# Performance work log

Measured on AMD Instinct MI355X. Metric: run time of the kernel, lower is better.

Reference implementation:

```python
import jax, jax.numpy as jnp
import numpy as np

B, S = 512, 128            # batch_size, seq_len
NE, ED = 8192, 128         # num_edges, edge_dim
DD, ND = 32, 8             # direction_dim, num directions
H, PL = 512, 5             # hidden_dim, pre_len


def setup_inputs() -> dict:
    key = jax.random.key(0)
    ks = jax.random.split(key, 18)
    stdv = 1.0 / np.sqrt(64.0)
    u = lambda k, shp: jax.random.uniform(k, shp, jnp.float32, -stdv, stdv)
    inputs = jax.random.randint(ks[0], (B, S), 1, NE + 1)          # 1..num_edges
    directions = jax.random.randint(ks[1], (B, S), 1, ND + 1)      # 1..direction
    goal = jax.random.randint(ks[2], (B,), 0, NE)                  # 0..num_edges-1
    loc_dlabels_matrix = jax.random.randint(ks[3], (NE, NE), 0, ND)
    pred_d_rand = jax.random.uniform(ks[4], (B, ND * PL))
    link_emb_w = jax.random.normal(ks[5], (NE + 1, ED)) * 0.02
    link_emb_w = link_emb_w.at[0].set(0.0)  # padding_idx=0
    dir_emb_w = jax.random.normal(ks[6], (ND + 1, DD)) * 0.02
    dir_emb_w = dir_emb_w.at[0].set(0.0)
    w_ih = u(ks[7], (4 * H, ED + DD)); b_ih = u(ks[8], (4 * H,))
    w_hh = u(ks[9], (4 * H, H));       b_hh = u(ks[10], (4 * H,))
    W1 = jax.random.normal(ks[11], (H, H)) * 0.02; b1 = jnp.zeros((H,))
    W2 = jax.random.normal(ks[12], (H, H)) * 0.02; b2 = jnp.zeros((H,))
    W3 = jax.random.normal(ks[13], (ND, H)) * 0.02; b3 = jnp.zeros((ND,))
    return dict(inputs=inputs, directions=directions, goal=goal,
                loc_dlabels_matrix=loc_dlabels_matrix, pred_d_rand=pred_d_rand,
                link_emb_w=link_emb_w, dir_emb_w=dir_emb_w,
                w_ih=w_ih, b_ih=b_ih, w_hh=w_hh, b_hh=b_hh,
                W1=W1, b1=b1, W2=W2, b2=b2, W3=W3, b3=b3)


def _lstm_final_h(x_tbc, w_ih, b_ih, w_hh, b_hh):
    # x_tbc: (S, B, E); returns final hidden state (B, H)
    h0 = jnp.zeros((x_tbc.shape[1], H), x_tbc.dtype)
    c0 = jnp.zeros_like(h0)
    def step(carry, x_t):
        h, c = carry
        gates = x_t @ w_ih.T + b_ih + h @ w_hh.T + b_hh   # (B, 4H)
        i, f, g, o = jnp.split(gates, 4, axis=-1)
        c = jax.nn.sigmoid(f) * c + jax.nn.sigmoid(i) * jnp.tanh(g)
        h = jax.nn.sigmoid(o) * jnp.tanh(c)
        return (h, c), None
    (h, _), _ = jax.lax.scan(step, (h0, c0), x_tbc)
    return h


def reference(inputs, directions, goal, loc_dlabels_matrix, pred_d_rand,
              link_emb_w, dir_emb_w, w_ih, b_ih, w_hh, b_hh,
              W1, b1, W2, b2, W3, b3):
    last_obs = inputs[:, -1]
    # goal_directions_label - 1 (class target, 0..ND-1)
    lbl = loc_dlabels_matrix[last_obs - 1, goal]
    # edge-sequence embeddings: (B, S, ED+DD)
    x = jnp.concatenate([link_emb_w[inputs], dir_emb_w[directions]], axis=-1)
    h = _lstm_final_h(jnp.swapaxes(x, 0, 1), w_ih, b_ih, w_hh, b_hh)
    # dropout is identity at inference
    z = jax.nn.relu(h @ W1.T + b1)
    z = jax.nn.relu(z @ W2.T + b2)
    logits = z @ W3.T + b3                                # (B, ND)
    pred_d_prob = jax.nn.log_softmax(logits, axis=1)
    # torch CrossEntropyLoss re-applies log_softmax to pred_d_prob (faithful)
    ls2 = jax.nn.log_softmax(pred_d_prob, axis=1)
    loss = -jnp.mean(ls2[jnp.arange(B), lbl]) * 5.0
    _, idx = jax.lax.top_k(pred_d_prob, 2)                # (B, 2)
    direction_correct = jnp.sum(((idx[:, 0] == lbl) | (idx[:, 1] == lbl)).astype(jnp.int32))
    le = link_emb_w[last_obs]                             # (B, ED)
    de = dir_emb_w[idx + 1]                               # (B, 2, DD) -- only meaningful if DD==ED? no: added below
    query = le + 0.5 * (de[:, 0, :] + de[:, 1, :]) if ED == DD else le + 0.0 * le
    # NOTE: original code adds direction embeddings to link embedding; requires edge_dim==direction_dim?
    # In the source both are projected into the same space implicitly; here edge_dim != direction_dim,
    # so pad direction embedding to edge_dim with zeros to keep the same math shapewise.
    de_pad = jnp.pad(0.5 * (de[:, 0, :] + de[:, 1, :]), ((0, 0), (0, ED - DD)))
    query = le + de_pad
    sim = query @ link_emb_w[1:, :].T                     # (B, NE)
    pred_hard = jnp.tile(sim, (1, PL))                    # (B, NE*PL)
    return pred_hard, pred_d_rand, loss, direction_correct
```

## Files before the change

kernel.cpp:

```cpp
#include <hip/hip_runtime.h>
#include <stdint.h>


typedef __attribute__((ext_vector_type(8))) short short8;
typedef __attribute__((ext_vector_type(4))) float f32x4;

__device__ __forceinline__ unsigned short f2bf(float f) {
  union { float f; unsigned u; } v; v.f = f;
  return (unsigned short)((v.u + 0x7fffu + ((v.u >> 16) & 1u)) >> 16);
}
__device__ __forceinline__ float bf2f(unsigned short h) {
  union { unsigned u; float f; } v; v.u = ((unsigned)h) << 16;
  return v.f;
}
__device__ __forceinline__ f32x4 MFMA(short8 a, short8 b, f32x4 c) {
  return __builtin_amdgcn_mfma_f32_16x16x32_bf16(a, b, c, 0, 0, 0);
}

__global__ __launch_bounds__(256) void k_prep(
    const int* __restrict__ inputs, const int* __restrict__ dirs,
    const float* __restrict__ link, const float* __restrict__ dire,
    const float* __restrict__ w_ih, const float* __restrict__ w_hh,
    const float* __restrict__ W1, const float* __restrict__ W2,
    const float* __restrict__ W3, const float* __restrict__ b_ih,
    const float* __restrict__ b_hh,
    unsigned short* __restrict__ xb, unsigned short* __restrict__ wihb,
    unsigned short* __restrict__ whhb, unsigned short* __restrict__ w1b,
    unsigned short* __restrict__ w2b, unsigned short* __restrict__ w3b,
    unsigned short* __restrict__ linkb, float* __restrict__ bias_sum)
{
  int64_t e = (int64_t)blockIdx.x * 256 + threadIdx.x;
  if (e < 10485760) {
    int ei = (int)e;
    int s = ei / 81920;
    int r = ei % 81920;
    int b = r / 160, k = r % 160;
    float v;
    if (k < 128) v = link[(int64_t)inputs[b*128 + s]*128 + k];
    else         v = dire[dirs[b*128 + s]*32 + (k - 128)];
    xb[ei] = f2bf(v);
    return;
  }
  e -= 10485760;
  if (e < 327680)  { wihb[e] = f2bf(w_ih[e]); return; }
  e -= 327680;
  if (e < 1048576) { whhb[e] = f2bf(w_hh[e]); return; }
  e -= 1048576;
  if (e < 262144)  { w1b[e] = f2bf(W1[e]); return; }
  e -= 262144;
  if (e < 262144)  { w2b[e] = f2bf(W2[e]); return; }
  e -= 262144;
  if (e < 4096)    { w3b[e] = f2bf(W3[e]); return; }
  e -= 4096;
  if (e < 1048704) { linkb[e] = f2bf(link[e]); return; }
  e -= 1048704;
  if (e < 2048)    { bias_sum[e] = b_ih[e] + b_hh[e]; return; }
}

__global__ __launch_bounds__(256) void k_gatesx(
    const unsigned short* __restrict__ xb, const unsigned short* __restrict__ wihb,
    const float* __restrict__ bias_sum, unsigned short* __restrict__ gx)
{
  const int jt1 = blockIdx.x;
  const int bt2 = blockIdx.y;
  const int s   = blockIdx.z;
  const int t = threadIdx.x, w = t >> 6, l = t & 63;

  __shared__ unsigned short Ash[16*64*8];
  __shared__ unsigned short Bsh[8*64*8];

  f32x4 acc[4][8];
#pragma unroll
  for (int ns = 0; ns < 8; ns++) {
    int dj = ns >> 2, g = ns & 3;
    int gcol = 512*g + 32*jt1 + 16*dj + (l & 15);
    float bv = bias_sum[gcol];
    f32x4 b4; b4[0] = bv; b4[1] = bv; b4[2] = bv; b4[3] = bv;
#pragma unroll
    for (int msl = 0; msl < 4; msl++) acc[msl][ns] = b4;
  }
  const unsigned short* xrow = xb + (int64_t)(s*512 + bt2*256)*160;

  for (int ch = 0; ch < 5; ch++) {
    __syncthreads();
#pragma unroll
    for (int i = 0; i < 4; i++) {
      int slot = t + 256*i;
      int ms = slot >> 6, ll = slot & 63;
      int row = 16*ms + (ll & 15);
      int k = 32*ch + 8*(ll >> 4);
      *(uint4*)&Ash[slot*8] = *(const uint4*)&xrow[row*160 + k];
    }
#pragma unroll
    for (int i = 0; i < 2; i++) {
      int slot = t + 256*i;
      int ns = slot >> 6, ll = slot & 63;
      int dj = ns >> 2, g = ns & 3;
      int gcol = 512*g + 32*jt1 + 16*dj + (ll & 15);
      int k = 32*ch + 8*(ll >> 4);
      *(uint4*)&Bsh[slot*8] = *(const uint4*)&wihb[gcol*160 + k];
    }
    __syncthreads();
    short8 Bf[8];
#pragma unroll
    for (int ns = 0; ns < 8; ns++) Bf[ns] = *(short8*)&Bsh[(ns*64 + l)*8];
#pragma unroll
    for (int msl = 0; msl < 4; msl++) {
      short8 Af = *(short8*)&Ash[((4*w + msl)*64 + l)*8];
#pragma unroll
      for (int ns = 0; ns < 8; ns++)
        acc[msl][ns] = MFMA(Af, Bf[ns], acc[msl][ns]);
    }
  }
#pragma unroll
  for (int msl = 0; msl < 4; msl++) {
    int ms1 = 4*w + msl;
    int brow0 = 256*bt2 + 16*ms1;
    int bt = brow0 >> 6;
    int ms2 = (brow0 >> 4) & 3;
    int mw = ms2 >> 1, mt = ms2 & 1;
#pragma unroll
    for (int ns = 0; ns < 8; ns++) {
      int dj = ns >> 2, g = ns & 3;
      int jt2 = 2*jt1 + dj;
      int nw = g >> 1, nt = g & 1;
      int w2 = 2*nw + mw;
      int64_t idx = ((((((int64_t)s*32 + jt2)*8 + bt)*4 + w2)*2 + mt)*2 + nt)*64 + l;
      f32x4 a = acc[msl][ns];
      uint2 pk;
      unsigned short* ps = (unsigned short*)&pk;
      ps[0] = f2bf(a[0]); ps[1] = f2bf(a[1]); ps[2] = f2bf(a[2]); ps[3] = f2bf(a[3]);
      *(uint2*)&gx[idx*4] = pk;
    }
  }
}

__global__ __launch_bounds__(256) void k_lstm_step(
    const unsigned short* __restrict__ hprev, unsigned short* __restrict__ hnext,
    float* __restrict__ cbuf, const unsigned short* __restrict__ whhb,
    const unsigned short* __restrict__ gx, int s)
{
  const int jt = blockIdx.x;
  const int bt = blockIdx.y;
  const int t = threadIdx.x, w = t >> 6, l = t & 63;
  const int mw = w & 1, nw = w >> 1;

  __shared__ unsigned short Ash[4*2*64*8];
  __shared__ unsigned short Bsh[4*2*64*8];
  __shared__ float gsh[64][68];

  f32x4 acc[2][2];
#pragma unroll
  for (int mt = 0; mt < 2; mt++)
#pragma unroll
  for (int nt = 0; nt < 2; nt++) {
    int64_t idx = ((((((int64_t)s*32 + jt)*8 + bt)*4 + w)*2 + mt)*2 + nt)*64 + l;
    uint2 raw = *(const uint2*)(gx + idx*4);
    const unsigned short* pk = (const unsigned short*)&raw;
    f32x4 v;
    v[0] = bf2f(pk[0]); v[1] = bf2f(pk[1]); v[2] = bf2f(pk[2]); v[3] = bf2f(pk[3]);
    acc[mt][nt] = v;
  }

  for (int ch = 0; ch < 8; ch++) {
    __syncthreads();
#pragma unroll
    for (int i = 0; i < 2; i++) {
      int slot = t + 256*i;
      int p = slot >> 6, ll = slot & 63;
      int ms = p >> 1, ks = p & 1;
      int row = 64*bt + 16*ms + (ll & 15);
      int k = 64*ch + 32*ks + 8*(ll >> 4);
      *(uint4*)&Ash[slot*8] = *(const uint4*)&hprev[row*512 + k];
    }
#pragma unroll
    for (int i = 0; i < 2; i++) {
      int slot = t + 256*i;
      int p = slot >> 6, ll = slot & 63;
      int ns = p >> 1, ks = p & 1;
      int gcol = 512*ns + 16*jt + (ll & 15);
      int k = 64*ch + 32*ks + 8*(ll >> 4);
      *(uint4*)&Bsh[slot*8] = *(const uint4*)&whhb[gcol*512 + k];
    }
    __syncthreads();
#pragma unroll
    for (int ks = 0; ks < 2; ks++) {
      short8 A0 = *(short8*)&Ash[(((2*mw+0)*2 + ks)*64 + l)*8];
      short8 A1 = *(short8*)&Ash[(((2*mw+1)*2 + ks)*64 + l)*8];
      short8 B0 = *(short8*)&Bsh[(((2*nw+0)*2 + ks)*64 + l)*8];
      short8 B1 = *(short8*)&Bsh[(((2*nw+1)*2 + ks)*64 + l)*8];
      acc[0][0] = MFMA(A0, B0, acc[0][0]);
      acc[0][1] = MFMA(A0, B1, acc[0][1]);
      acc[1][0] = MFMA(A1, B0, acc[1][0]);
      acc[1][1] = MFMA(A1, B1, acc[1][1]);
    }
  }

#pragma unroll
  for (int mt = 0; mt < 2; mt++)
#pragma unroll
  for (int nt = 0; nt < 2; nt++) {
    int cb = 32*nw + 16*nt + (l & 15);
    int rb = 32*mw + 16*mt + (l >> 4)*4;
    f32x4 a = acc[mt][nt];
#pragma unroll
    for (int r = 0; r < 4; r++) gsh[rb + r][cb] = a[r];
  }
  __syncthreads();

  {
    int m = t >> 2, u0 = (t & 3)*4;
    int b = 64*bt + m;
    int j0 = 16*jt + u0;
    float* cp = cbuf + b*512 + j0;
    f32x4 c = *(f32x4*)cp;
    f32x4 cn;
    uint2 hv;
    unsigned short* hs = (unsigned short*)&hv;
#pragma unroll
    for (int i2 = 0; i2 < 4; i2++) {
      float gi = gsh[m][ 0 + u0 + i2];
      float gf = gsh[m][16 + u0 + i2];
      float gg = gsh[m][32 + u0 + i2];
      float go = gsh[m][48 + u0 + i2];
      float ii = 1.f/(1.f + expf(-gi));
      float ff = 1.f/(1.f + expf(-gf));
      float g2 = tanhf(gg);
      float oo = 1.f/(1.f + expf(-go));
      float cv = ff*c[i2] + ii*g2;
      cn[i2] = cv;
      hs[i2] = f2bf(oo * tanhf(cv));
    }
    *(f32x4*)cp = cn;
    *(uint2*)&hnext[b*512 + j0] = hv;
  }
}

__global__ __launch_bounds__(256, 1) void k_lstm_all(
    unsigned short* __restrict__ hb0, unsigned short* __restrict__ hb1,
    const unsigned short* __restrict__ whhb,
    const unsigned short* __restrict__ wihb,
    const unsigned short* __restrict__ xb,
    const float* __restrict__ bias_sum,
    unsigned int* __restrict__ flags)
{
  const int jt = blockIdx.x;
  const int bt = blockIdx.y;
  const int t = threadIdx.x, w = t >> 6, l = t & 63;
  const int mw = w & 1, nw = w >> 1;

  __shared__ unsigned short Ash[8*2*4*64*8];
  __shared__ float gsh[64][68];

  unsigned int* gf = flags + bt*32;

  short8 Bw[8][2][2];
#pragma unroll
  for (int ch = 0; ch < 8; ch++)
#pragma unroll
  for (int ks = 0; ks < 2; ks++)
#pragma unroll
  for (int nsl = 0; nsl < 2; nsl++) {
    int ns = 2*nw + nsl;
    int gcol = 512*ns + 16*jt + (l & 15);
    int k = 64*ch + 32*ks + 8*(l >> 4);
    Bw[ch][ks][nsl] = *(const short8*)&whhb[(int64_t)gcol*512 + k];
  }
  short8 Wx[5][2];
#pragma unroll
  for (int ch = 0; ch < 5; ch++)
#pragma unroll
  for (int nsl = 0; nsl < 2; nsl++) {
    int ns = 2*nw + nsl;
    int gcol = 512*ns + 16*jt + (l & 15);
    int k = 32*ch + 8*(l >> 4);
    Wx[ch][nsl] = *(const short8*)&wihb[(int64_t)gcol*160 + k];
  }
  float bias_b[2];
#pragma unroll
  for (int nt = 0; nt < 2; nt++) {
    int g = 2*nw + nt;
    bias_b[nt] = bias_sum[512*g + 16*jt + (l & 15)];
  }

  float creg[4] = {0.f, 0.f, 0.f, 0.f};
  const int m = t >> 2, u0 = (t & 3)*4;
  const int bgl = 64*bt + m;
  const int j0 = 16*jt + u0;

  short8 xf[2][5];
#pragma unroll
  for (int mt = 0; mt < 2; mt++)
#pragma unroll
  for (int ch = 0; ch < 5; ch++) {
    int row = 64*bt + 32*mw + 16*mt + (l & 15);
    int k = 32*ch + 8*(l >> 4);
    xf[mt][ch] = *(const short8*)&xb[(int64_t)(0*512 + row)*160 + k];
  }

  for (int s = 0; s < 128; s++) {
    const unsigned short* hp = (s & 1) ? hb1 : hb0;
    unsigned short* hn = (s & 1) ? hb0 : hb1;

    uint2 gxr[2][2];
#pragma unroll
    for (int mt = 0; mt < 2; mt++)
#pragma unroll
    for (int nt = 0; nt < 2; nt++) {
      f32x4 a;
      a[0] = bias_b[nt]; a[1] = bias_b[nt]; a[2] = bias_b[nt]; a[3] = bias_b[nt];
#pragma unroll
      for (int ch = 0; ch < 5; ch++)
        a = MFMA(xf[mt][ch], Wx[ch][nt], a);
      unsigned short* ps = (unsigned short*)&gxr[mt][nt];
      ps[0] = f2bf(a[0]); ps[1] = f2bf(a[1]); ps[2] = f2bf(a[2]); ps[3] = f2bf(a[3]);
    }

    {
      int sn = (s + 1 < 128) ? s + 1 : 127;
#pragma unroll
      for (int mt = 0; mt < 2; mt++)
#pragma unroll
      for (int ch = 0; ch < 5; ch++) {
        int row = 64*bt + 32*mw + 16*mt + (l & 15);
        int k = 32*ch + 8*(l >> 4);
        xf[mt][ch] = *(const short8*)&xb[(int64_t)(sn*512 + row)*160 + k];
      }
    }

    if (s > 0) {
      if (w == 0) {
        unsigned tgt = (unsigned)s;
        for (;;) {
          unsigned v = __hip_atomic_load(&gf[l & 31], __ATOMIC_RELAXED,
                                         __HIP_MEMORY_SCOPE_AGENT);
          if (__all((int)(v >= tgt))) break;
          __builtin_amdgcn_s_sleep(2);
        }
      }
      __syncthreads();
    }

#pragma unroll
    for (int i = 0; i < 16; i++) {
      int p = w*16 + i;
      int ms = p & 3, ks = (p >> 2) & 1, ch = p >> 3;
      int row = 64*bt + 16*ms + (l & 15);
      int k = 64*ch + 32*ks + 8*(l >> 4);
      const unsigned long long* src =
          (const unsigned long long*)(hp + (int64_t)row*512 + k);
      unsigned long long d0 = __hip_atomic_load(src,     __ATOMIC_RELAXED,
                                                __HIP_MEMORY_SCOPE_AGENT);
      unsigned long long d1 = __hip_atomic_load(src + 1, __ATOMIC_RELAXED,
                                                __HIP_MEMORY_SCOPE_AGENT);
      unsigned long long tmp[2] = {d0, d1};
      *(uint4*)&Ash[(p*64 + l)*8] = *(const uint4*)tmp;
    }
    __syncthreads();

    f32x4 acc[2][2];
#pragma unroll
    for (int mt = 0; mt < 2; mt++)
#pragma unroll
    for (int nt = 0; nt < 2; nt++) {
      const unsigned short* pk = (const unsigned short*)&gxr[mt][nt];
      f32x4 v;
      v[0] = bf2f(pk[0]); v[1] = bf2f(pk[1]); v[2] = bf2f(pk[2]); v[3] = bf2f(pk[3]);
      acc[mt][nt] = v;
    }

#pragma unroll
    for (int ch = 0; ch < 8; ch++)
#pragma unroll
    for (int ks = 0; ks < 2; ks++) {
      short8 A0 = *(short8*)&Ash[((ch*8 + ks*4 + 2*mw + 0)*64 + l)*8];
      short8 A1 = *(short8*)&Ash[((ch*8 + ks*4 + 2*mw + 1)*64 + l)*8];
      acc[0][0] = MFMA(A0, Bw[ch][ks][0], acc[0][0]);
      acc[0][1] = MFMA(A0, Bw[ch][ks][1], acc[0][1]);
      acc[1][0] = MFMA(A1, Bw[ch][ks][0], acc[1][0]);
      acc[1][1] = MFMA(A1, Bw[ch][ks][1], acc[1][1]);
    }

#pragma unroll
    for (int mt = 0; mt < 2; mt++)
#pragma unroll
    for (int nt = 0; nt < 2; nt++) {
      int cb = 32*nw + 16*nt + (l & 15);
      int rb = 32*mw + 16*mt + (l >> 4)*4;
      f32x4 a = acc[mt][nt];
#pragma unroll
      for (int r = 0; r < 4; r++) gsh[rb + r][cb] = a[r];
    }
    __syncthreads();

    {
      union { unsigned short hs[4]; unsigned long long v; } hv;
#pragma unroll
      for (int i2 = 0; i2 < 4; i2++) {
        float gi = gsh[m][ 0 + u0 + i2];
        float gf2 = gsh[m][16 + u0 + i2];
        float gg = gsh[m][32 + u0 + i2];
        float go = gsh[m][48 + u0 + i2];
        float ii = 1.f/(1.f + expf(-gi));
        float ff = 1.f/(1.f + expf(-gf2));
        float g2 = tanhf(gg);
        float oo = 1.f/(1.f + expf(-go));
        float cv = ff*creg[i2] + ii*g2;
        creg[i2] = cv;
        hv.hs[i2] = f2bf(oo * tanhf(cv));
      }
      __hip_atomic_store((unsigned long long*)&hn[(int64_t)bgl*512 + j0], hv.v,
                         __ATOMIC_RELAXED, __HIP_MEMORY_SCOPE_AGENT);
    }

    __syncthreads();
    if (t == 0) {
      asm volatile("s_waitcnt vmcnt(0)" ::: "memory");
      __hip_atomic_store(&gf[jt], (unsigned)(s + 1), __ATOMIC_RELAXED,
                         __HIP_MEMORY_SCOPE_AGENT);
    }
  }
}

template<int MODE>
__global__ __launch_bounds__(256) void k_gemm(
    const unsigned short* __restrict__ A, int lda,
    const unsigned short* __restrict__ Bm, int ldb, int nreal,
    const float* __restrict__ bias,
    void* __restrict__ outp, int ldo, int nchunks)
{
  const int bX = blockIdx.x, bY = blockIdx.y;
  const int t = threadIdx.x, w = t >> 6, l = t & 63;
  const int mw = w & 1, nw = w >> 1;
  __shared__ unsigned short Ash[4*2*64*8];
  __shared__ unsigned short Bsh[4*2*64*8];

  f32x4 acc[2][2];
  f32x4 z; z[0] = 0.f; z[1] = 0.f; z[2] = 0.f; z[3] = 0.f;
  acc[0][0] = z; acc[0][1] = z; acc[1][0] = z; acc[1][1] = z;

  for (int ch = 0; ch < nchunks; ch++) {
    __syncthreads();
#pragma unroll
    for (int i = 0; i < 2; i++) {
      int slot = t + 256*i;
      int p = slot >> 6, ll = slot & 63;
      int ms = p >> 1, ks = p & 1;
      int row = 64*bY + 16*ms + (ll & 15);
      int k = 64*ch + 32*ks + 8*(ll >> 4);
      *(uint4*)&Ash[slot*8] = *(const uint4*)&A[(int64_t)row*lda + k];
    }
#pragma unroll
    for (int i = 0; i < 2; i++) {
      int slot = t + 256*i;
      int p = slot >> 6, ll = slot & 63;
      int ns = p >> 1, ks = p & 1;
      int row = 64*bX + 16*ns + (ll & 15);
      if (row >= nreal) row = nreal - 1;
      int k = 64*ch + 32*ks + 8*(ll >> 4);
      *(uint4*)&Bsh[slot*8] = *(const uint4*)&Bm[(int64_t)row*ldb + k];
    }
    __syncthreads();
#pragma unroll
    for (int ks = 0; ks < 2; ks++) {
      short8 A0 = *(short8*)&Ash[(((2*mw+0)*2 + ks)*64 + l)*8];
      short8 A1 = *(short8*)&Ash[(((2*mw+1)*2 + ks)*64 + l)*8];
      short8 B0 = *(short8*)&Bsh[(((2*nw+0)*2 + ks)*64 + l)*8];
      short8 B1 = *(short8*)&Bsh[(((2*nw+1)*2 + ks)*64 + l)*8];
      acc[0][0] = MFMA(A0, B0, acc[0][0]);
      acc[0][1] = MFMA(A0, B1, acc[0][1]);
      acc[1][0] = MFMA(A1, B0, acc[1][0]);
      acc[1][1] = MFMA(A1, B1, acc[1][1]);
    }
  }

#pragma unroll
  for (int mt = 0; mt < 2; mt++)
#pragma unroll
  for (int nt = 0; nt < 2; nt++) {
    int n = 64*bX + 32*nw + 16*nt + (l & 15);
    int rb = 64*bY + 32*mw + 16*mt + (l >> 4)*4;
    f32x4 a = acc[mt][nt];
    if (MODE == 0) {
      float bv = bias[n];
#pragma unroll
      for (int r = 0; r < 4; r++) {
        float v = a[r] + bv; v = v > 0.f ? v : 0.f;
        ((unsigned short*)outp)[(int64_t)(rb + r)*ldo + n] = f2bf(v);
      }
    } else if (MODE == 1) {
      if (n < nreal) {
        float bv = bias[n];
#pragma unroll
        for (int r = 0; r < 4; r++)
          ((float*)outp)[(int64_t)(rb + r)*ldo + n] = a[r] + bv;
      }
    } else {
#pragma unroll
      for (int r = 0; r < 4; r++) {
        float v = a[r];
        float* o = (float*)outp + (int64_t)(rb + r)*40960 + n;
#pragma unroll
        for (int p5 = 0; p5 < 5; p5++) o[p5*8192] = v;
      }
    }
  }
}

__global__ __launch_bounds__(256) void k_head(
    const float* __restrict__ logits, const int* __restrict__ inputs,
    const int* __restrict__ goal, const int* __restrict__ ldm,
    const float* __restrict__ link, const float* __restrict__ dire,
    const float* __restrict__ pdr, unsigned short* __restrict__ qb,
    float* __restrict__ out)
{
  const int blk = blockIdx.x, t = threadIdx.x;
  __shared__ int idxsh[64][2];
  __shared__ float redf[256];
  __shared__ int redi[256];

  if (t < 64) {
    int b = 64*blk + t;
    float v[8];
#pragma unroll
    for (int i = 0; i < 8; i++) v[i] = logits[b*8 + i];
    int i0 = 0; float m0 = v[0];
#pragma unroll
    for (int i = 1; i < 8; i++) if (v[i] > m0) { m0 = v[i]; i0 = i; }
    int i1 = -1; float m1 = -3.4e38f;
#pragma unroll
    for (int i = 0; i < 8; i++) if (i != i0 && v[i] > m1) { m1 = v[i]; i1 = i; }
    idxsh[t][0] = i0; idxsh[t][1] = i1;
  }
  __syncthreads();
  {
    int rl = t >> 2, kc = (t & 3) * 32;
    int b = 64*blk + rl;
    int last = inputs[b*128 + 127];
    const float* le = link + (int64_t)last*128 + kc;
    int i0 = idxsh[rl][0], i1 = idxsh[rl][1];
    unsigned short q[32] __attribute__((aligned(16)));
#pragma unroll
    for (int k = 0; k < 32; k++) {
      float v = le[k];
      if (kc == 0) v += 0.5f*(dire[(i0+1)*32 + k] + dire[(i1+1)*32 + k]);
      q[k] = f2bf(v);
    }
    uint4* dst = (uint4*)&qb[b*128 + kc];
#pragma unroll
    for (int x = 0; x < 4; x++) dst[x] = ((uint4*)q)[x];
  }
  if (blk == 0) {
    float lsum = 0.f; int csum = 0;
    for (int rr = t; rr < 512; rr += 256) {
      float v[8];
#pragma unroll
      for (int i = 0; i < 8; i++) v[i] = logits[rr*8 + i];
      float mx = v[0];
#pragma unroll
      for (int i = 1; i < 8; i++) mx = v[i] > mx ? v[i] : mx;
      float se = 0.f;
#pragma unroll
      for (int i = 0; i < 8; i++) se += expf(v[i] - mx);
      float lse = logf(se);
      int last = inputs[rr*128 + 127];
      int lbl = ldm[(int64_t)(last - 1)*8192 + goal[rr]];
      lsum += v[lbl] - mx - lse;
      int i0 = 0; float m0 = v[0];
#pragma unroll
      for (int i = 1; i < 8; i++) if (v[i] > m0) { m0 = v[i]; i0 = i; }
      int i1 = -1; float m1 = -3.4e38f;
#pragma unroll
      for (int i = 0; i < 8; i++) if (i != i0 && v[i] > m1) { m1 = v[i]; i1 = i; }
      if (i0 == lbl || i1 == lbl) csum++;
    }
    redf[t] = lsum; redi[t] = csum;
    __syncthreads();
    for (int o2 = 128; o2 > 0; o2 >>= 1) {
      if (t < o2) { redf[t] += redf[t + o2]; redi[t] += redi[t + o2]; }
      __syncthreads();
    }
    if (t == 0) {
      out[20992000] = -redf[0] / 512.f * 5.f;
      out[20992001] = (float)redi[0];
    }
  }
  for (int i = 0; i < 10; i++) {
    int idx = blk*2560 + t*10 + i;
    out[20971520 + idx] = pdr[idx];
  }
}

extern "C" void kernel_launch(void* const* d_in, const int* in_sizes, int n_in,
                              void* d_out, int out_size, void* d_ws, size_t ws_size,
                              hipStream_t stream)
{
  const int* inputs = (const int*)d_in[0];
  const int* dirs   = (const int*)d_in[1];
  const int* goal   = (const int*)d_in[2];
  const int* ldm    = (const int*)d_in[3];
  const float* pdr  = (const float*)d_in[4];
  const float* link = (const float*)d_in[5];
  const float* dire = (const float*)d_in[6];
  const float* w_ih = (const float*)d_in[7];
  const float* b_ih = (const float*)d_in[8];
  const float* w_hh = (const float*)d_in[9];
  const float* b_hh = (const float*)d_in[10];
  const float* W1   = (const float*)d_in[11];
  const float* b1   = (const float*)d_in[12];
  const float* W2   = (const float*)d_in[13];
  const float* b2   = (const float*)d_in[14];
  const float* W3   = (const float*)d_in[15];
  const float* b3   = (const float*)d_in[16];
  float* out = (float*)d_out;

  char* wsp = (char*)d_ws;
  size_t off = 0;
  auto alloc = [&](size_t bytes) { char* p = wsp + off; off += (bytes + 255) & ~(size_t)255; return p; };
  unsigned short* xb    = (unsigned short*)alloc(10485760ull*2);
  unsigned short* wihb  = (unsigned short*)alloc(327680ull*2);
  unsigned short* whhb  = (unsigned short*)alloc(1048576ull*2);
  unsigned short* w1b   = (unsigned short*)alloc(262144ull*2);
  unsigned short* w2b   = (unsigned short*)alloc(262144ull*2);
  unsigned short* w3b   = (unsigned short*)alloc(4096ull*2);
  unsigned short* linkb = (unsigned short*)alloc(1048704ull*2);
  float* bias_sum       = (float*)alloc(2048ull*4);
  unsigned short* gxb   = (unsigned short*)alloc(134217728ull*2);
  unsigned short* hb0   = (unsigned short*)alloc(262144ull*2);
  unsigned short* hb1   = (unsigned short*)alloc(262144ull*2);
  float* cbuf           = (float*)alloc(262144ull*4);
  unsigned short* z1b   = (unsigned short*)alloc(262144ull*2);
  unsigned short* z2b   = (unsigned short*)alloc(262144ull*2);
  float* logits         = (float*)alloc(4096ull*4);
  unsigned short* qb    = (unsigned short*)alloc(65536ull*2);
  unsigned int* flags   = (unsigned int*)alloc(4096);

  hipMemsetAsync(hb0, 0, 262144ull*2, stream);
  hipMemsetAsync(flags, 0, 4096, stream);

  k_prep<<<52505, 256, 0, stream>>>(inputs, dirs, link, dire, w_ih, w_hh, W1, W2, W3,
                                    b_ih, b_hh, xb, wihb, whhb, w1b, w2b, w3b, linkb, bias_sum);

  {
    unsigned short* a0 = hb0; unsigned short* a1 = hb1;
    const unsigned short* a2 = whhb; const unsigned short* a3 = wihb;
    const unsigned short* a4 = xb; const float* a5 = bias_sum;
    unsigned int* a6 = flags;
    void* kargs[7] = { &a0, &a1, &a2, &a3, &a4, &a5, &a6 };
    hipError_t ce = hipLaunchCooperativeKernel((const void*)k_lstm_all,
                                               dim3(32,8,1), dim3(256,1,1),
                                               kargs, 0, stream);
    if (ce != hipSuccess) {
      k_gatesx<<<dim3(16,2,128), 256, 0, stream>>>(xb, wihb, bias_sum, gxb);
      hipMemsetAsync(cbuf, 0, 262144ull*4, stream);
      for (int s = 0; s < 128; s++) {
        const unsigned short* hp = (s & 1) ? hb1 : hb0;
        unsigned short* hn = (s & 1) ? hb0 : hb1;
        k_lstm_step<<<dim3(32,8), 256, 0, stream>>>(hp, hn, cbuf, whhb, gxb, s);
      }
    }
  }
  k_gemm<0><<<dim3(8,8), 256, 0, stream>>>(hb0, 512, w1b, 512, 512, b1, z1b, 512, 8);
  k_gemm<0><<<dim3(8,8), 256, 0, stream>>>(z1b, 512, w2b, 512, 512, b2, z2b, 512, 8);
  k_gemm<1><<<dim3(1,8), 256, 0, stream>>>(z2b, 512, w3b, 512, 8, b3, logits, 8, 8);
  k_head<<<8, 256, 0, stream>>>(logits, inputs, goal, ldm, link, dire, pdr, qb, out);
  k_gemm<2><<<dim3(128,8), 256, 0, stream>>>(qb, 128, linkb + 128, 128, 8192, nullptr, out, 0, 2);
}
```

Measured before the change: 1.598 ms.

## Map LSTM batch tiles to XCDs so step sync stays within one chiplet

Each persistent LSTM block reads its hardware XCC ID at startup and claims a slot through atomic counters, so the 32 blocks that exchange hidden state for one batch tile all sit on the same XCD. When the mapping is uniform, the per-step flag polling, hidden-state loads and stores switch from agent-scope atomics to plain volatile accesses, aiming for cheaper cross-block communication through the shared L2. If the mapping is not uniform, the old blockIdx mapping and atomics are used, and timeouts are added to the spin loops. The risks are correctness, because volatile accesses may not be coherent across CUs, plus an extra startup barrier and a skipped wait when a timeout fires.

```diff
diff --git a/kernel.cpp b/kernel.cpp
--- a/kernel.cpp
+++ b/kernel.cpp
@@ -242,17 +242,45 @@
     const unsigned short* __restrict__ wihb,
     const unsigned short* __restrict__ xb,
     const float* __restrict__ bias_sum,
-    unsigned int* __restrict__ flags)
+    unsigned int* __restrict__ flags,
+    unsigned int* __restrict__ cnt)
 {
-  const int jt = blockIdx.x;
-  const int bt = blockIdx.y;
   const int t = threadIdx.x, w = t >> 6, l = t & 63;
   const int mw = w & 1, nw = w >> 1;
 
   __shared__ unsigned short Ash[8*2*4*64*8];
   __shared__ float gsh[64][68];
-
-  unsigned int* gf = flags + bt*32;
+  __shared__ int roster[3];
+
+  if (t == 0) {
+    unsigned xcd;
+    asm volatile("s_getreg_b32 %0, hwreg(HW_REG_XCC_ID)" : "=s"(xcd));
+    xcd &= 7u;
+    unsigned slot = __hip_atomic_fetch_add(&cnt[xcd], 1u, __ATOMIC_RELAXED,
+                                           __HIP_MEMORY_SCOPE_AGENT);
+    __hip_atomic_fetch_add(&cnt[8], 1u, __ATOMIC_RELEASE,
+                           __HIP_MEMORY_SCOPE_AGENT);
+    bool ok = true;
+    for (int it2 = 0; ; ++it2) {
+      if (__hip_atomic_load(&cnt[8], __ATOMIC_ACQUIRE,
+                            __HIP_MEMORY_SCOPE_AGENT) >= 256u) break;
+      if (it2 > 5000000) { ok = false; break; }
+      __builtin_amdgcn_s_sleep(2);
+    }
+    bool uniform = ok;
+    for (int x2 = 0; x2 < 8; x2++)
+      if (__hip_atomic_load(&cnt[x2], __ATOMIC_RELAXED,
+                            __HIP_MEMORY_SCOPE_AGENT) != 32u) uniform = false;
+    if (uniform) { roster[0] = (int)slot; roster[1] = (int)xcd; roster[2] = 1; }
+    else { roster[0] = (int)(blockIdx.x & 31); roster[1] = (int)(blockIdx.x >> 5);
+           roster[2] = 0; }
+  }
+  __syncthreads();
+  const int jt  = roster[0];
+  const int bt  = roster[1];
+  const bool loc = roster[2] != 0;
+
+  unsigned int* gf = flags + bt*64;
 
   short8 Bw[8][2][2];
 #pragma unroll
@@ -287,6 +315,7 @@
   const int m = t >> 2, u0 = (t & 3)*4;
   const int bgl = 64*bt + m;
   const int j0 = 16*jt + u0;
+  int bad = 0;
 
   short8 xf[2][5];
 #pragma unroll
@@ -329,32 +358,51 @@
     }
 
     if (s > 0) {
-      if (w == 0) {
+      if (w == 0 && !bad) {
         unsigned tgt = (unsigned)s;
-        for (;;) {
-          unsigned v = __hip_atomic_load(&gf[l & 31], __ATOMIC_RELAXED,
+        for (int it2 = 0; ; ++it2) {
+          unsigned v;
+          if (loc) v = *(volatile const unsigned*)&gf[l & 31];
+          else     v = __hip_atomic_load(&gf[l & 31], __ATOMIC_RELAXED,
                                          __HIP_MEMORY_SCOPE_AGENT);
           if (__all((int)(v >= tgt))) break;
-          __builtin_amdgcn_s_sleep(2);
+          if (it2 > 1000000) { bad = 1; break; }
+          __builtin_amdgcn_s_sleep(1);
         }
       }
       __syncthreads();
     }
 
-#pragma unroll
-    for (int i = 0; i < 16; i++) {
-      int p = w*16 + i;
-      int ms = p & 3, ks = (p >> 2) & 1, ch = p >> 3;
-      int row = 64*bt + 16*ms + (l & 15);
-      int k = 64*ch + 32*ks + 8*(l >> 4);
-      const unsigned long long* src =
-          (const unsigned long long*)(hp + (int64_t)row*512 + k);
-      unsigned long long d0 = __hip_atomic_load(src,     __ATOMIC_RELAXED,
-                                                __HIP_MEMORY_SCOPE_AGENT);
-      unsigned long long d1 = __hip_atomic_load(src + 1, __ATOMIC_RELAXED,
-                                                __HIP_MEMORY_SCOPE_AGENT);
-      unsigned long long tmp[2] = {d0, d1};
-      *(uint4*)&Ash[(p*64 + l)*8] = *(const uint4*)tmp;
+    if (loc) {
+#pragma unroll
+      for (int i = 0; i < 16; i++) {
+        int p = w*16 + i;
+        int ms = p & 3, ks = (p >> 2) & 1, ch = p >> 3;
+        int row = 64*bt + 16*ms + (l & 15);
+        int k = 64*ch + 32*ks + 8*(l >> 4);
+        const volatile unsigned long long* src =
+            (const volatile unsigned long long*)(hp + (int64_t)row*512 + k);
+        unsigned long long d0 = src[0];
+        unsigned long long d1 = src[1];
+        unsigned long long tmp[2] = {d0, d1};
+        *(uint4*)&Ash[(p*64 + l)*8] = *(const uint4*)tmp;
+      }
+    } else {
+#pragma unroll
+      for (int i = 0; i < 16; i++) {
+        int p = w*16 + i;
+        int ms = p & 3, ks = (p >> 2) & 1, ch = p >> 3;
+        int row = 64*bt + 16*ms + (l & 15);
+        int k = 64*ch + 32*ks + 8*(l >> 4);
+        const unsigned long long* src =
+            (const unsigned long long*)(hp + (int64_t)row*512 + k);
+        unsigned long long d0 = __hip_atomic_load(src,     __ATOMIC_RELAXED,
+                                                  __HIP_MEMORY_SCOPE_AGENT);
+        unsigned long long d1 = __hip_atomic_load(src + 1, __ATOMIC_RELAXED,
+                                                  __HIP_MEMORY_SCOPE_AGENT);
+        unsigned long long tmp[2] = {d0, d1};
+        *(uint4*)&Ash[(p*64 + l)*8] = *(const uint4*)tmp;
+      }
     }
     __syncthreads();
 
@@ -409,15 +457,19 @@
         creg[i2] = cv;
         hv.hs[i2] = f2bf(oo * tanhf(cv));
       }
-      __hip_atomic_store((unsigned long long*)&hn[(int64_t)bgl*512 + j0], hv.v,
-                         __ATOMIC_RELAXED, __HIP_MEMORY_SCOPE_AGENT);
+      if (loc)
+        *(unsigned long long*)&hn[(int64_t)bgl*512 + j0] = hv.v;
+      else
+        __hip_atomic_store((unsigned long long*)&hn[(int64_t)bgl*512 + j0],
+                           hv.v, __ATOMIC_RELAXED, __HIP_MEMORY_SCOPE_AGENT);
     }
 
     __syncthreads();
     if (t == 0) {
       asm volatile("s_waitcnt vmcnt(0)" ::: "memory");
-      __hip_atomic_store(&gf[jt], (unsigned)(s + 1), __ATOMIC_RELAXED,
-                         __HIP_MEMORY_SCOPE_AGENT);
+      if (loc) *(volatile unsigned*)&gf[jt] = (unsigned)(s + 1);
+      else __hip_atomic_store(&gf[jt], (unsigned)(s + 1), __ATOMIC_RELAXED,
+                              __HIP_MEMORY_SCOPE_AGENT);
     }
   }
 }
@@ -634,9 +686,11 @@
   float* logits         = (float*)alloc(4096ull*4);
   unsigned short* qb    = (unsigned short*)alloc(65536ull*2);
   unsigned int* flags   = (unsigned int*)alloc(4096);
+  unsigned int* cnt     = (unsigned int*)alloc(256);
 
   hipMemsetAsync(hb0, 0, 262144ull*2, stream);
   hipMemsetAsync(flags, 0, 4096, stream);
+  hipMemsetAsync(cnt, 0, 256, stream);
 
   k_prep<<<52505, 256, 0, stream>>>(inputs, dirs, link, dire, w_ih, w_hh, W1, W2, W3,
                                     b_ih, b_hh, xb, wihb, whhb, w1b, w2b, w3b, linkb, bias_sum);
@@ -645,10 +699,10 @@
     unsigned short* a0 = hb0; unsigned short* a1 = hb1;
     const unsigned short* a2 = whhb; const unsigned short* a3 = wihb;
     const unsigned short* a4 = xb; const float* a5 = bias_sum;
-    unsigned int* a6 = flags;
-    void* kargs[7] = { &a0, &a1, &a2, &a3, &a4, &a5, &a6 };
+    unsigned int* a6 = flags; unsigned int* a7 = cnt;
+    void* kargs[8] = { &a0, &a1, &a2, &a3, &a4, &a5, &a6, &a7 };
     hipError_t ce = hipLaunchCooperativeKernel((const void*)k_lstm_all,
-                                               dim3(32,8,1), dim3(256,1,1),
+                                               dim3(256,1,1), dim3(256,1,1),
                                                kargs, 0, stream);
     if (ce != hipSuccess) {
       k_gatesx<<<dim3(16,2,128), 256, 0, stream>>>(xb, wihb, bias_sum, gxb);
```

Measured after the change: 1.481 ms. 7.3% less time.
